# Kernel optimization log

Measured on AMD Instinct MI355X. Metric: run time of the kernel, lower is better.

Reference implementation:

```python
import jax, jax.numpy as jnp
import numpy as np

EPS = 1e-5  # torch LayerNorm default


def setup_inputs() -> dict:
    key = jax.random.key(0)
    k1, k2, k3 = jax.random.split(key, 3)
    B, C, O, M, H, Wd = 4, 64, 64, 4, 384, 384
    x = jax.random.normal(k1, (B, C, H, Wd), dtype=jnp.float32)
    # DNM_W is [M, out, in, 1, 1] -> flattened 1x1 conv weights [M, out, in]
    W = jax.random.uniform(k2, (M, O, C), dtype=jnp.float32)
    q = jax.random.uniform(k3, (1,), dtype=jnp.float32)
    gamma = jnp.ones((C,), jnp.float32)   # LayerNorm weight (norm1)
    beta = jnp.zeros((C,), jnp.float32)   # LayerNorm bias (norm1)
    return {"x": x, "W": W, "q": q, "gamma": gamma, "beta": beta}


def reference(x, W, q, gamma, beta):
    # x: [B, C, H, W]; LayerNorm over channel dim (module permutes to NHWC first)
    xt = jnp.transpose(x, (0, 2, 3, 1))            # [B, H, W, C]
    mu = jnp.mean(xt, axis=-1, keepdims=True)
    var = jnp.var(xt, axis=-1, keepdims=True)      # biased, matches torch
    xn = (xt - mu) * jax.lax.rsqrt(var + EPS) * gamma + beta
    # M parallel 1x1 convs == per-pixel matmuls, batched into one einsum
    y = jnp.einsum('bhwc,moc->mbhwo', xn, W)       # [M, B, H, W, O]
    out = jnp.sum(jnp.maximum(y - q, 0.0), axis=0) # relu(conv - q), sum over M
    return jnp.transpose(out, (0, 3, 1, 2))        # [B, O, H, W]
```

## Files before the change

### kernel.cpp

```cpp
#include <hip/hip_runtime.h>
#include <hip/hip_bf16.h>

typedef __attribute__((ext_vector_type(8))) short short8;
typedef __attribute__((ext_vector_type(4))) float f32x4;

#define HWPIX 147456
#define NC 64
#define NO 64
#define NM 4
#define EPSV 1e-5f

static __device__ __forceinline__ unsigned short f2bf(float f) {
    unsigned int u = __float_as_uint(f);
    u += 0x7fffu + ((u >> 16) & 1u);
    return (unsigned short)(u >> 16);
}
static __device__ __forceinline__ float bf2f(unsigned short h) {
    return __uint_as_float(((unsigned int)h) << 16);
}

#define BAR() do { asm volatile("s_waitcnt lgkmcnt(0)" ::: "memory"); \
                   __builtin_amdgcn_s_barrier();                      \
                   asm volatile("" ::: "memory"); } while (0)

__global__ __launch_bounds__(256) void dnm_fused(
    const float* __restrict__ x, const float* __restrict__ Wg,
    const float* __restrict__ qp, const float* __restrict__ gamma,
    const float* __restrict__ beta, float* __restrict__ out)
{
    __shared__ __align__(16) unsigned char lds[2][8192];

    const int tid = threadIdx.x;
    const int wv  = tid >> 6;
    const int ln  = tid & 63;
    const int p16 = ln & 15;
    const int g4  = ln >> 4;

    const int bid = blockIdx.x;
    const int b       = bid / 576;
    const int pixbase = (bid % 576) * 256;

    const float qv = qp[0];
    const float q4 = 4.0f * qv;

    f32x4 gA[2], gB[2], bA[2], bB[2];
#pragma unroll
    for (int ch = 0; ch < 2; ++ch) {
        gA[ch] = *(const f32x4*)(gamma + ch * 32 + g4 * 8);
        gB[ch] = *(const f32x4*)(gamma + ch * 32 + g4 * 8 + 4);
        bA[ch] = *(const f32x4*)(beta  + ch * 32 + g4 * 8);
        bB[ch] = *(const f32x4*)(beta  + ch * 32 + g4 * 8 + 4);
    }
    short8 wh[NM][2], wl[NM][2];
    float bias[NM];
#pragma unroll
    for (int m = 0; m < NM; ++m) {
        float bsum = 0.f;
#pragma unroll
        for (int ch = 0; ch < 2; ++ch) {
            const float* wp = Wg + ((m * NO + (wv * 16 + p16)) * NC + ch * 32 + g4 * 8);
            f32x4 a = *(const f32x4*)(wp);
            f32x4 c = *(const f32x4*)(wp + 4);
            float f[8]  = {a[0], a[1], a[2], a[3], c[0], c[1], c[2], c[3]};
            float gg[8] = {gA[ch][0], gA[ch][1], gA[ch][2], gA[ch][3],
                           gB[ch][0], gB[ch][1], gB[ch][2], gB[ch][3]};
            float bb[8] = {bA[ch][0], bA[ch][1], bA[ch][2], bA[ch][3],
                           bB[ch][0], bB[ch][1], bB[ch][2], bB[ch][3]};
#pragma unroll
            for (int j = 0; j < 8; ++j) {
                bsum += bb[j] * f[j];
                float wq = gg[j] * f[j];
                unsigned short h  = f2bf(wq);
                unsigned short lo = f2bf(wq - bf2f(h));
                wh[m][ch][j] = (short)h;
                wl[m][ch][j] = (short)lo;
            }
        }
        bsum += __shfl_xor(bsum, 16);
        bsum += __shfl_xor(bsum, 32);
        bias[m] = bsum;
    }

    const float* xpl = x + (size_t)b * NC * HWPIX + pixbase + wv * 16 + p16
                         + (size_t)(g4 * 16) * HWPIX;
    float* const outw = out + (size_t)b * NO * HWPIX
                            + (size_t)(wv * 16 + p16) * HWPIX + pixbase;

    const int r  = wv * 16 + p16;
    const int rk = r & 7;

    float xv[16];
#pragma unroll
    for (int i = 0; i < 16; ++i) xv[i] = xpl[(size_t)i * HWPIX];

#pragma unroll 1
    for (int it = 0; it < 4; ++it) {
        unsigned char* buf = lds[it & 1];

        {
            float s1 = 0.f, s2 = 0.f;
#pragma unroll
            for (int i = 0; i < 16; ++i) { s1 += xv[i]; s2 += xv[i] * xv[i]; }
            s1 += __shfl_xor(s1, 16);  s2 += __shfl_xor(s2, 16);
            s1 += __shfl_xor(s1, 32);  s2 += __shfl_xor(s2, 32);
            const float mu  = s1 * (1.f / 64.f);
            const float var = s2 * (1.f / 64.f) - mu * mu;
            const float rs  = rsqrtf(var + EPSV);
            short8 hi0, hi1;
#pragma unroll
            for (int i = 0; i < 16; ++i) {
                float xn = (xv[i] - mu) * rs;
                unsigned short h = f2bf(xn);
                if (i < 8) hi0[i] = (short)h; else hi1[i - 8] = (short)h;
            }
            const int s0 = g4 * 2;
            *(short8*)(buf + r * 128 + (((s0    ) ^ rk) << 4)) = hi0;
            *(short8*)(buf + r * 128 + (((s0 + 1) ^ rk) << 4)) = hi1;
        }
        BAR();

        if (it < 3) {
            const float* xp = xpl + (it + 1) * 64;
#pragma unroll
            for (int i = 0; i < 16; ++i) xv[i] = xp[(size_t)i * HWPIX];
        }

#pragma unroll 1
        for (int ps = 0; ps < 4; ++ps) {
            const int row = ps * 16 + p16;
            const int rwk = row & 7;
            short8 ah[2];
#pragma unroll
            for (int ch = 0; ch < 2; ++ch) {
                const int slot = ch * 4 + g4;
                ah[ch] = *(const short8*)(buf + row * 128 + ((slot ^ rwk) << 4));
            }
            f32x4 acc[NM];
#pragma unroll
            for (int m = 0; m < NM; ++m) {
                f32x4 a = {bias[m], bias[m], bias[m], bias[m]};
#pragma unroll
                for (int ch = 0; ch < 2; ++ch) {
                    a = __builtin_amdgcn_mfma_f32_16x16x32_bf16(ah[ch], wh[m][ch], a, 0, 0, 0);
                    a = __builtin_amdgcn_mfma_f32_16x16x32_bf16(ah[ch], wl[m][ch], a, 0, 0, 0);
                }
                acc[m] = a;
            }
            f32x4 v;
#pragma unroll
            for (int rr = 0; rr < 4; ++rr) {
                v[rr] = (fmaxf(acc[0][rr], qv) + fmaxf(acc[1][rr], qv))
                      + (fmaxf(acc[2][rr], qv) + fmaxf(acc[3][rr], qv)) - q4;
            }
            *(f32x4*)(outw + it * 64 + ps * 16 + g4 * 4) = v;
        }
    }
}

extern "C" void kernel_launch(void* const* d_in, const int* in_sizes, int n_in,
                              void* d_out, int out_size, void* d_ws, size_t ws_size,
                              hipStream_t stream) {
    const float* x     = (const float*)d_in[0];
    const float* Wg    = (const float*)d_in[1];
    const float* q     = (const float*)d_in[2];
    const float* gamma = (const float*)d_in[3];
    const float* beta  = (const float*)d_in[4];
    float* out = (float*)d_out;

    dnm_fused<<<dim3(2304), dim3(256), 0, stream>>>(x, Wg, q, gamma, beta, out);
}
```

Measured before the change: 83.88 us.

## Use packed bf16 convert instruction and double pixels per block

Replaces the manual round-to-nearest bf16 conversion with the hardware v_cvt_pk_bf16_f32 instruction, which converts two floats per instruction. This applies both to the hi/lo weight split and to the normalized activations. It also halves the grid so each block handles 512 pixels over 8 iterations, spreading the per-block weight setup across more work. The cost is fewer blocks to fill the GPU and a longer serial loop in each block.

```diff
diff --git a/kernel.cpp b/kernel.cpp
--- a/kernel.cpp
+++ b/kernel.cpp
@@ -3,6 +3,7 @@
 
 typedef __attribute__((ext_vector_type(8))) short short8;
 typedef __attribute__((ext_vector_type(4))) float f32x4;
+typedef __attribute__((ext_vector_type(4))) unsigned int u32x4;
 
 #define HWPIX 147456
 #define NC 64
@@ -10,13 +11,13 @@
 #define NM 4
 #define EPSV 1e-5f
 
-static __device__ __forceinline__ unsigned short f2bf(float f) {
-    unsigned int u = __float_as_uint(f);
-    u += 0x7fffu + ((u >> 16) & 1u);
-    return (unsigned short)(u >> 16);
+static __device__ __forceinline__ unsigned int cvt_pk(float a, float b) {
+    unsigned int r;
+    asm("v_cvt_pk_bf16_f32 %0, %1, %2" : "=v"(r) : "v"(a), "v"(b));
+    return r;
 }
-static __device__ __forceinline__ float bf2f(unsigned short h) {
-    return __uint_as_float(((unsigned int)h) << 16);
+static __device__ __forceinline__ float asf(unsigned int u) {
+    return __uint_as_float(u);
 }
 
 #define BAR() do { asm volatile("s_waitcnt lgkmcnt(0)" ::: "memory"); \
@@ -37,8 +38,8 @@
     const int g4  = ln >> 4;
 
     const int bid = blockIdx.x;
-    const int b       = bid / 576;
-    const int pixbase = (bid % 576) * 256;
+    const int b       = bid / 288;
+    const int pixbase = (bid % 288) * 512;
 
     const float qv = qp[0];
     const float q4 = 4.0f * qv;
@@ -66,15 +67,23 @@
                            gB[ch][0], gB[ch][1], gB[ch][2], gB[ch][3]};
             float bb[8] = {bA[ch][0], bA[ch][1], bA[ch][2], bA[ch][3],
                            bB[ch][0], bB[ch][1], bB[ch][2], bB[ch][3]};
+            float wq[8];
 #pragma unroll
             for (int j = 0; j < 8; ++j) {
                 bsum += bb[j] * f[j];
-                float wq = gg[j] * f[j];
-                unsigned short h  = f2bf(wq);
-                unsigned short lo = f2bf(wq - bf2f(h));
-                wh[m][ch][j] = (short)h;
-                wl[m][ch][j] = (short)lo;
+                wq[j] = gg[j] * f[j];
             }
+            u32x4 hu, lu;
+#pragma unroll
+            for (int p = 0; p < 4; ++p) {
+                unsigned int h = cvt_pk(wq[2*p], wq[2*p+1]);
+                float r0 = wq[2*p]   - asf(h << 16);
+                float r1 = wq[2*p+1] - asf(h & 0xffff0000u);
+                hu[p] = h;
+                lu[p] = cvt_pk(r0, r1);
+            }
+            wh[m][ch] = __builtin_bit_cast(short8, hu);
+            wl[m][ch] = __builtin_bit_cast(short8, lu);
         }
         bsum += __shfl_xor(bsum, 16);
         bsum += __shfl_xor(bsum, 32);
@@ -94,7 +103,7 @@
     for (int i = 0; i < 16; ++i) xv[i] = xpl[(size_t)i * HWPIX];
 
 #pragma unroll 1
-    for (int it = 0; it < 4; ++it) {
+    for (int it = 0; it < 8; ++it) {
         unsigned char* buf = lds[it & 1];
 
         {
@@ -106,20 +115,19 @@
             const float mu  = s1 * (1.f / 64.f);
             const float var = s2 * (1.f / 64.f) - mu * mu;
             const float rs  = rsqrtf(var + EPSV);
-            short8 hi0, hi1;
+            u32x4 h0, h1;
 #pragma unroll
-            for (int i = 0; i < 16; ++i) {
-                float xn = (xv[i] - mu) * rs;
-                unsigned short h = f2bf(xn);
-                if (i < 8) hi0[i] = (short)h; else hi1[i - 8] = (short)h;
+            for (int p = 0; p < 4; ++p) {
+                h0[p] = cvt_pk((xv[2*p]     - mu) * rs, (xv[2*p+1] - mu) * rs);
+                h1[p] = cvt_pk((xv[8+2*p]   - mu) * rs, (xv[9+2*p] - mu) * rs);
             }
             const int s0 = g4 * 2;
-            *(short8*)(buf + r * 128 + (((s0    ) ^ rk) << 4)) = hi0;
-            *(short8*)(buf + r * 128 + (((s0 + 1) ^ rk) << 4)) = hi1;
+            *(u32x4*)(buf + r * 128 + (((s0    ) ^ rk) << 4)) = h0;
+            *(u32x4*)(buf + r * 128 + (((s0 + 1) ^ rk) << 4)) = h1;
         }
         BAR();
 
-        if (it < 3) {
+        if (it < 7) {
             const float* xp = xpl + (it + 1) * 64;
 #pragma unroll
             for (int i = 0; i < 16; ++i) xv[i] = xp[(size_t)i * HWPIX];
@@ -167,5 +175,5 @@
     const float* beta  = (const float*)d_in[4];
     float* out = (float*)d_out;
 
-    dnm_fused<<<dim3(2304), dim3(256), 0, stream>>>(x, Wg, q, gamma, beta, out);
+    dnm_fused<<<dim3(1152), dim3(256), 0, stream>>>(x, Wg, q, gamma, beta, out);
 }
```

Result: faster. 75.74 us (-9.7%).
